# Performance work log

Hardware: AMD Instinct MI355X
Metric: run time of the kernel (lower is better)

Reference implementation:

```python
import jax, jax.numpy as jnp
import numpy as np

# config matching init_kwargs
WS = 7          # window side -> N = 49 tokens
NUM_HEADS = 8
DIM = 256
N = WS * WS     # 49
NW = 64         # windows per image (56x56 feature map / 7x7 windows)
B = 64          # images
B_ = B * NW     # 4096 window-batches


def _relative_position_index():
    # exact replica of the numpy construction in __init__
    coords_h = np.arange(WS)
    coords_w = np.arange(WS)
    coords = np.stack(np.meshgrid(coords_h, coords_w, indexing='ij'))  # (2, WS, WS)
    coords_flatten = coords.reshape(2, -1)                             # (2, N)
    rel = coords_flatten[:, :, None] - coords_flatten[:, None, :]      # (2, N, N)
    rel = rel.transpose(1, 2, 0)                                       # (N, N, 2)
    rel[:, :, 0] += WS - 1
    rel[:, :, 1] += WS - 1
    rel[:, :, 0] *= 2 * WS - 1
    return rel.sum(-1).astype(np.int32)                                # (N, N) in [0, 169)


def setup_inputs() -> dict:
    key = jax.random.key(0)
    k1, k2, k3 = jax.random.split(key, 3)
    x = jax.random.normal(k1, (B_, N, DIM), dtype=jnp.float32)
    bias_table = jax.random.normal(k2, (169, NUM_HEADS), dtype=jnp.float32) * 0.02
    mask = jax.random.normal(k3, (NW, N, N), dtype=jnp.float32)
    rel_index = jnp.asarray(_relative_position_index())
    return {"x": x, "bias_table": bias_table, "mask": mask, "rel_index": rel_index}


def reference(x, bias_table, mask, rel_index):
    B_, n, C = x.shape
    head_dim = C // NUM_HEADS
    scale = head_dim ** -0.5
    # NOTE: original call() uses x_qkv[0] for q, k AND v (qkv Dense never applied)
    qkv = x.reshape(B_, n, NUM_HEADS, head_dim).transpose(0, 2, 1, 3)  # (B_, H, N, hd)
    attn = jnp.einsum('bhid,bhjd->bhij', qkv * scale, qkv)             # (B_, H, N, N)
    # gathered relative-position bias: (N*N, H) -> (H, N, N)
    bias = bias_table[rel_index.reshape(-1)].reshape(n, n, NUM_HEADS).transpose(2, 0, 1)
    attn = attn + bias[None]
    # additive window mask: (nW, N, N) broadcast over batch and heads
    nW = mask.shape[0]
    attn = attn.reshape(B_ // nW, nW, NUM_HEADS, n, n) + mask[None, :, None]
    attn = jax.nn.softmax(attn.reshape(B_, NUM_HEADS, n, n), axis=-1)
    out = jnp.einsum('bhij,bhjd->bhid', attn, qkv)                     # (B_, H, N, hd)
    return out.transpose(0, 2, 1, 3).reshape(B_, n, C)
```

## Files before the change

### kernel.cpp

```cpp
#include <hip/hip_runtime.h>
#include <hip/hip_bf16.h>

typedef float f32x4 __attribute__((ext_vector_type(4)));
typedef short s16x8 __attribute__((ext_vector_type(8)));
typedef unsigned int u32;

#define LOG2E 1.4426950408889634f
#define NEGINF (-1e30f)

__device__ __forceinline__ unsigned short f2bf(float f) {
    __hip_bfloat16 h = __float2bfloat16(f);
    unsigned short u;
    __builtin_memcpy(&u, &h, 2);
    return u;
}

__global__ void fuse_bias_mask(const float* __restrict__ bias_table,
                               const float* __restrict__ mask,
                               const int*   __restrict__ rel_index,
                               float*       __restrict__ fused) {
    int tid = blockIdx.x * 256 + threadIdx.x;
    const int total = 512 * 2401;
    if (tid >= total) return;
    int wh  = tid / 2401;
    int rem = tid - wh * 2401;
    int c   = rem / 49;
    int w = wh >> 3, h = wh & 7;
    int idx = rel_index[rem];
    float v = (mask[w * 2401 + rem] + bias_table[idx * 8 + h]) * LOG2E;
    fused[((long)wh * 49 + c) * 52 + (rem - c * 49)] = v;
}

template<bool FUSED>
__global__ __launch_bounds__(256, 3)
void win_attn(const float* __restrict__ x,
              const float* __restrict__ bias_table,
              const float* __restrict__ mask,
              const int*   __restrict__ rel_index,
              const float* __restrict__ fused,
              float*       __restrict__ out) {
    __shared__ char Plds[4][8192];
    const int tid  = threadIdx.x;
    const int wav  = tid >> 6;
    const int lane = tid & 63;
    const int li   = lane & 15;
    const int g    = lane >> 4;
    char* P = &Plds[wav][0];
    const float scale2 = 0.17677669529663689f * LOG2E;

    const int b0 = blockIdx.x * 2;

    f32x4 raw[4][2];

    auto issue_raw = [&](int task) {
        int it = task >> 1, hh = task & 1;
        int b = b0 + it, h = wav * 2 + hh;
        const float* xh = x + (long)b * (49 * 256) + h * 32;
        #pragma unroll
        for (int t = 0; t < 4; ++t) {
            int row = t * 16 + li;
            if (row < 49) {
                const f32x4* p = (const f32x4*)(xh + (long)row * 256 + g * 8);
                raw[t][0] = p[0];
                raw[t][1] = p[1];
            } else {
                raw[t][0] = f32x4{0.f, 0.f, 0.f, 0.f};
                raw[t][1] = f32x4{0.f, 0.f, 0.f, 0.f};
            }
        }
    };

    issue_raw(0);

    #pragma unroll 1
    for (int task = 0; task < 4; ++task) {
        const int it = task >> 1, hh = task & 1;
        const int b = b0 + it, h = wav * 2 + hh, w = b & 63;
        const float* xh = x + (long)b * (49 * 256) + h * 32;

        float vraw[2][2][8];
        #pragma unroll
        for (int nd = 0; nd < 2; ++nd)
            #pragma unroll
            for (int kt = 0; kt < 2; ++kt) {
                int d = li + 16 * nd;
                #pragma unroll
                for (int jj = 0; jj < 8; ++jj) {
                    int j = 32 * kt + 8 * g + jj;
                    vraw[nd][kt][jj] = (j < 49) ? xh[(long)j * 256 + d] : 0.f;
                }
            }

        s16x8 Fh[4], Fl[4];
        #pragma unroll
        for (int t = 0; t < 4; ++t) {
            u32 hp[4], lp[4];
            #pragma unroll
            for (int pq = 0; pq < 4; ++pq) {
                float f0 = raw[t][pq >> 1][(pq & 1) * 2 + 0];
                float f1 = raw[t][pq >> 1][(pq & 1) * 2 + 1];
                u32 u0 = __float_as_uint(f0), u1 = __float_as_uint(f1);
                hp[pq] = (u0 >> 16) | (u1 & 0xFFFF0000u);
                float r0 = f0 - __uint_as_float(u0 & 0xFFFF0000u);
                float r1 = f1 - __uint_as_float(u1 & 0xFFFF0000u);
                lp[pq] = (u32)f2bf(r0) | ((u32)f2bf(r1) << 16);
            }
            __builtin_memcpy(&Fh[t], hp, 16);
            __builtin_memcpy(&Fl[t], lp, 16);
        }

        s16x8 Vf[2][2];
        #pragma unroll
        for (int nd = 0; nd < 2; ++nd)
            #pragma unroll
            for (int kt = 0; kt < 2; ++kt) {
                s16x8 vv;
                #pragma unroll
                for (int jj = 0; jj < 8; ++jj)
                    vv[jj] = (short)f2bf(vraw[nd][kt][jj]);
                Vf[nd][kt] = vv;
            }

        if (task < 3) issue_raw(task + 1);

        const int wh = w * 8 + h;
        #pragma unroll
        for (int nc = 0; nc < 4; ++nc) {
            __builtin_amdgcn_s_setprio(1);
            f32x4 a[4];
            #pragma unroll
            for (int mr = 0; mr < 4; ++mr) {
                f32x4 t = f32x4{0.f, 0.f, 0.f, 0.f};
                t = __builtin_amdgcn_mfma_f32_16x16x32_bf16(Fh[mr], Fh[nc], t, 0, 0, 0);
                t = __builtin_amdgcn_mfma_f32_16x16x32_bf16(Fh[mr], Fl[nc], t, 0, 0, 0);
                t = __builtin_amdgcn_mfma_f32_16x16x32_bf16(Fl[mr], Fh[nc], t, 0, 0, 0);
                a[mr] = t;
            }
            __builtin_amdgcn_s_setprio(0);

            int c = li + 16 * nc;
            int cidx = min(c, 48);
            if (FUSED) {
                const float* fb = fused + ((long)wh * 49 + cidx) * 52;
                #pragma unroll
                for (int mr = 0; mr < 3; ++mr) {
                    f32x4 tt = *(const f32x4*)(fb + 16 * mr + 4 * g);
                    #pragma unroll
                    for (int i = 0; i < 4; ++i)
                        a[mr][i] = a[mr][i] * scale2 + tt[i];
                }
                float t48 = fb[48];
                a[3][0] = (g == 0) ? a[3][0] * scale2 + t48 : NEGINF;
                a[3][1] = NEGINF; a[3][2] = NEGINF; a[3][3] = NEGINF;
            } else {
                const int base = cidx * 49;
                #pragma unroll
                for (int mr = 0; mr < 3; ++mr)
                    #pragma unroll
                    for (int i = 0; i < 4; ++i) {
                        int r = 16 * mr + 4 * g + i;
                        float bm = (mask[w * 2401 + base + r]
                                    + bias_table[rel_index[base + r] * 8 + h]) * LOG2E;
                        a[mr][i] = a[mr][i] * scale2 + bm;
                    }
                float bm48 = (mask[w * 2401 + base + 48]
                              + bias_table[rel_index[base + 48] * 8 + h]) * LOG2E;
                a[3][0] = (g == 0) ? a[3][0] * scale2 + bm48 : NEGINF;
                a[3][1] = NEGINF; a[3][2] = NEGINF; a[3][3] = NEGINF;
            }

            float m = fmaxf(fmaxf(fmaxf(a[0][0], a[0][1]), fmaxf(a[0][2], a[0][3])),
                            fmaxf(fmaxf(a[1][0], a[1][1]), fmaxf(a[1][2], a[1][3])));
            m = fmaxf(m, fmaxf(fmaxf(fmaxf(a[2][0], a[2][1]), fmaxf(a[2][2], a[2][3])),
                               fmaxf(fmaxf(a[3][0], a[3][1]), fmaxf(a[3][2], a[3][3]))));
            m = fmaxf(m, __shfl_xor(m, 16));
            m = fmaxf(m, __shfl_xor(m, 32));

            float s = 0.f;
            #pragma unroll
            for (int mr = 0; mr < 4; ++mr)
                #pragma unroll
                for (int i = 0; i < 4; ++i) {
                    float p = __builtin_amdgcn_exp2f(a[mr][i] - m);
                    a[mr][i] = p;
                    s += p;
                }
            s += __shfl_xor(s, 16);
            s += __shfl_xor(s, 32);
            float sinv = __builtin_amdgcn_rcpf(s);

            char* rowp = P + c * 128;
            unsigned sw = ((unsigned)(c & 7)) << 4;
            #pragma unroll
            for (int mr = 0; mr < 4; ++mr) {
                u32 p0 = (u32)f2bf(a[mr][0] * sinv) | ((u32)f2bf(a[mr][1] * sinv) << 16);
                u32 p1 = (u32)f2bf(a[mr][2] * sinv) | ((u32)f2bf(a[mr][3] * sinv) << 16);
                uint2 v; v.x = p0; v.y = p1;
                *(uint2*)(rowp + (((unsigned)(32 * mr + 8 * g)) ^ sw)) = v;
            }
        }

        f32x4 o[4][2];
        #pragma unroll
        for (int mc = 0; mc < 4; ++mc)
            #pragma unroll
            for (int nd = 0; nd < 2; ++nd) o[mc][nd] = f32x4{0.f, 0.f, 0.f, 0.f};
        __builtin_amdgcn_s_setprio(1);
        #pragma unroll
        for (int mc = 0; mc < 4; ++mc) {
            int c2 = li + 16 * mc;
            char* rowp = P + c2 * 128;
            unsigned sw = ((unsigned)(c2 & 7)) << 4;
            #pragma unroll
            for (int kt = 0; kt < 2; ++kt) {
                s16x8 pa = *(const s16x8*)(rowp + (((unsigned)(64 * kt + 16 * g)) ^ sw));
                #pragma unroll
                for (int nd = 0; nd < 2; ++nd)
                    o[mc][nd] = __builtin_amdgcn_mfma_f32_16x16x32_bf16(pa, Vf[nd][kt], o[mc][nd], 0, 0, 0);
            }
        }
        __builtin_amdgcn_s_setprio(0);

        float* ob = out + (long)b * (49 * 256) + h * 32;
        #pragma unroll
        for (int mc = 0; mc < 4; ++mc) {
            int cbase = 16 * mc + 4 * g;
            #pragma unroll
            for (int i = 0; i < 4; ++i) {
                int crow = cbase + i;
                if (crow < 49) {
                    #pragma unroll
                    for (int nd = 0; nd < 2; ++nd)
                        __builtin_nontemporal_store(o[mc][nd][i],
                            &ob[(long)crow * 256 + 16 * nd + li]);
                }
            }
        }
    }
}

extern "C" void kernel_launch(void* const* d_in, const int* in_sizes, int n_in,
                              void* d_out, int out_size, void* d_ws, size_t ws_size,
                              hipStream_t stream) {
    const float* x          = (const float*)d_in[0];
    const float* bias_table = (const float*)d_in[1];
    const float* mask       = (const float*)d_in[2];
    const int*   rel_index  = (const int*)d_in[3];
    float* out   = (float*)d_out;
    float* fused = (float*)d_ws;

    const size_t need = (size_t)512 * 49 * 52 * 4;
    if (ws_size >= need) {
        const int total = 512 * 2401;
        fuse_bias_mask<<<(total + 255) / 256, 256, 0, stream>>>(bias_table, mask, rel_index, fused);
        win_attn<true><<<2048, 256, 0, stream>>>(x, bias_table, mask, rel_index, fused, out);
    } else {
        win_attn<false><<<2048, 256, 0, stream>>>(x, bias_table, mask, rel_index, nullptr, out);
    }
}
```

Before: 434.0 us.

## One window per block, packed bf16 conversion, drop cross-task prefetch

Each block now handles a single window batch (4096 blocks instead of 2048 with two windows each), and the software prefetch of the next task's x tile is removed. Float-to-bf16 conversions use the packed v_cvt_pk_bf16_f32 instruction instead of scalar conversions. The P tile in LDS shrinks to 49 rows, padded rows are skipped on write and clamped on read, and output stores become regular instead of nontemporal. The aim is more parallelism, smaller LDS for occupancy and cheaper conversions, at the cost of losing load/compute overlap inside a block.

```diff
diff --git a/kernel.cpp b/kernel.cpp
--- a/kernel.cpp
+++ b/kernel.cpp
@@ -8,11 +8,10 @@
 #define LOG2E 1.4426950408889634f
 #define NEGINF (-1e30f)
 
-__device__ __forceinline__ unsigned short f2bf(float f) {
-    __hip_bfloat16 h = __float2bfloat16(f);
-    unsigned short u;
-    __builtin_memcpy(&u, &h, 2);
-    return u;
+__device__ __forceinline__ u32 cvt_pk_bf16(float a, float b) {
+    u32 r;
+    asm("v_cvt_pk_bf16_f32 %0, %1, %2" : "=v"(r) : "v"(a), "v"(b));
+    return r;
 }
 
 __global__ void fuse_bias_mask(const float* __restrict__ bias_table,
@@ -39,7 +38,7 @@
               const int*   __restrict__ rel_index,
               const float* __restrict__ fused,
               float*       __restrict__ out) {
-    __shared__ char Plds[4][8192];
+    __shared__ char Plds[4][49 * 128];
     const int tid  = threadIdx.x;
     const int wav  = tid >> 6;
     const int lane = tid & 63;
@@ -48,14 +47,16 @@
     char* P = &Plds[wav][0];
     const float scale2 = 0.17677669529663689f * LOG2E;
 
-    const int b0 = blockIdx.x * 2;
-
-    f32x4 raw[4][2];
-
-    auto issue_raw = [&](int task) {
-        int it = task >> 1, hh = task & 1;
-        int b = b0 + it, h = wav * 2 + hh;
-        const float* xh = x + (long)b * (49 * 256) + h * 32;
+    const int b = blockIdx.x;
+    const int w = b & 63;
+    const float* xb = x + (long)b * (49 * 256);
+
+    #pragma unroll 1
+    for (int hh = 0; hh < 2; ++hh) {
+        const int h = wav * 2 + hh;
+        const float* xh = xb + h * 32;
+
+        f32x4 raw[4][2];
         #pragma unroll
         for (int t = 0; t < 4; ++t) {
             int row = t * 16 + li;
@@ -68,15 +69,6 @@
                 raw[t][1] = f32x4{0.f, 0.f, 0.f, 0.f};
             }
         }
-    };
-
-    issue_raw(0);
-
-    #pragma unroll 1
-    for (int task = 0; task < 4; ++task) {
-        const int it = task >> 1, hh = task & 1;
-        const int b = b0 + it, h = wav * 2 + hh, w = b & 63;
-        const float* xh = x + (long)b * (49 * 256) + h * 32;
 
         float vraw[2][2][8];
         #pragma unroll
@@ -103,7 +95,7 @@
                 hp[pq] = (u0 >> 16) | (u1 & 0xFFFF0000u);
                 float r0 = f0 - __uint_as_float(u0 & 0xFFFF0000u);
                 float r1 = f1 - __uint_as_float(u1 & 0xFFFF0000u);
-                lp[pq] = (u32)f2bf(r0) | ((u32)f2bf(r1) << 16);
+                lp[pq] = cvt_pk_bf16(r0, r1);
             }
             __builtin_memcpy(&Fh[t], hp, 16);
             __builtin_memcpy(&Fl[t], lp, 16);
@@ -114,14 +106,12 @@
         for (int nd = 0; nd < 2; ++nd)
             #pragma unroll
             for (int kt = 0; kt < 2; ++kt) {
-                s16x8 vv;
-                #pragma unroll
-                for (int jj = 0; jj < 8; ++jj)
-                    vv[jj] = (short)f2bf(vraw[nd][kt][jj]);
-                Vf[nd][kt] = vv;
-            }
-
-        if (task < 3) issue_raw(task + 1);
+                u32 vp[4];
+                #pragma unroll
+                for (int p = 0; p < 4; ++p)
+                    vp[p] = cvt_pk_bf16(vraw[nd][kt][2 * p], vraw[nd][kt][2 * p + 1]);
+                __builtin_memcpy(&Vf[nd][kt], vp, 16);
+            }
 
         const int wh = w * 8 + h;
         #pragma unroll
@@ -189,14 +179,16 @@
             s += __shfl_xor(s, 32);
             float sinv = __builtin_amdgcn_rcpf(s);
 
-            char* rowp = P + c * 128;
-            unsigned sw = ((unsigned)(c & 7)) << 4;
-            #pragma unroll
-            for (int mr = 0; mr < 4; ++mr) {
-                u32 p0 = (u32)f2bf(a[mr][0] * sinv) | ((u32)f2bf(a[mr][1] * sinv) << 16);
-                u32 p1 = (u32)f2bf(a[mr][2] * sinv) | ((u32)f2bf(a[mr][3] * sinv) << 16);
-                uint2 v; v.x = p0; v.y = p1;
-                *(uint2*)(rowp + (((unsigned)(32 * mr + 8 * g)) ^ sw)) = v;
+            if (c <= 48) {
+                char* rowp = P + c * 128;
+                u32 sw = ((u32)(c & 7)) << 4;
+                #pragma unroll
+                for (int mr = 0; mr < 4; ++mr) {
+                    uint2 v;
+                    v.x = cvt_pk_bf16(a[mr][0] * sinv, a[mr][1] * sinv);
+                    v.y = cvt_pk_bf16(a[mr][2] * sinv, a[mr][3] * sinv);
+                    *(uint2*)(rowp + (((u32)(32 * mr + 8 * g)) ^ sw)) = v;
+                }
             }
         }
 
@@ -208,12 +200,12 @@
         __builtin_amdgcn_s_setprio(1);
         #pragma unroll
         for (int mc = 0; mc < 4; ++mc) {
-            int c2 = li + 16 * mc;
-            char* rowp = P + c2 * 128;
-            unsigned sw = ((unsigned)(c2 & 7)) << 4;
+            int cr = min(li + 16 * mc, 48);
+            char* rowp = P + cr * 128;
+            u32 sw = ((u32)(cr & 7)) << 4;
             #pragma unroll
             for (int kt = 0; kt < 2; ++kt) {
-                s16x8 pa = *(const s16x8*)(rowp + (((unsigned)(64 * kt + 16 * g)) ^ sw));
+                s16x8 pa = *(const s16x8*)(rowp + (((u32)(64 * kt + 16 * g)) ^ sw));
                 #pragma unroll
                 for (int nd = 0; nd < 2; ++nd)
                     o[mc][nd] = __builtin_amdgcn_mfma_f32_16x16x32_bf16(pa, Vf[nd][kt], o[mc][nd], 0, 0, 0);
@@ -231,8 +223,7 @@
                 if (crow < 49) {
                     #pragma unroll
                     for (int nd = 0; nd < 2; ++nd)
-                        __builtin_nontemporal_store(o[mc][nd][i],
-                            &ob[(long)crow * 256 + 16 * nd + li]);
+                        ob[(long)crow * 256 + 16 * nd + li] = o[mc][nd][i];
                 }
             }
         }
@@ -253,8 +244,8 @@
     if (ws_size >= need) {
         const int total = 512 * 2401;
         fuse_bias_mask<<<(total + 255) / 256, 256, 0, stream>>>(bias_table, mask, rel_index, fused);
-        win_attn<true><<<2048, 256, 0, stream>>>(x, bias_table, mask, rel_index, fused, out);
+        win_attn<true><<<4096, 256, 0, stream>>>(x, bias_table, mask, rel_index, fused, out);
     } else {
-        win_attn<false><<<2048, 256, 0, stream>>>(x, bias_table, mask, rel_index, nullptr, out);
+        win_attn<false><<<4096, 256, 0, stream>>>(x, bias_table, mask, rel_index, nullptr, out);
     }
 }
```

After: 379.0 us. -12.7%, faster.
